# Kernel optimization log

Hardware: AMD Instinct MI355X
Metric: run time of the kernel (lower is better)

The kernel has to match this reference:

```python
import jax, jax.numpy as jnp
import numpy as np
from jax import lax

B, C, T, D, H, W = 1, 8, 8, 24, 48, 48
KT = 3  # temporal kernel taps (module's time loop == valid forward conv, stride 1, pad 0)
KS = 3  # spatial kernel size
S = 2   # spatial stride of the transposed conv
P = 1   # spatial padding of the transposed conv


def setup_inputs() -> dict:
    key = jax.random.key(0)
    kx, kw = jax.random.split(key)
    x = jax.random.normal(kx, (B, C, T, D, H, W), dtype=jnp.float32)
    # torch layout (out_channels, in_channels, kT, kD, kH, kW); the module assigns the
    # slice weight[:, :, i] directly as ConvTranspose3d.weight, so at runtime dim0 acts
    # as the transpose-conv INPUT-channel dim (works because in_ch == out_ch).
    fan_in = C * KT * KS ** 3
    bound = float(1.0 / np.sqrt(fan_in))
    weight = jax.random.uniform(kw, (C, C, KT, KS, KS, KS), dtype=jnp.float32,
                                minval=-bound, maxval=bound)
    return {"x": x, "weight": weight}


def _convT3d(x5, wt):
    # x5: [N, Cin, D, H, W]; wt: ConvTranspose3d weight laid out [Cin, Cout, kD, kH, kW].
    # Transposed conv == forward conv with spatially flipped kernel, swapped I/O dims,
    # lhs dilation = stride, per-side padding = dil*(k-1) - p.
    rhs = jnp.flip(wt, axis=(2, 3, 4)).transpose(1, 0, 2, 3, 4)  # [Cout, Cin, k, k, k]
    pad = KS - 1 - P
    return lax.conv_general_dilated(
        x5, rhs,
        window_strides=(1, 1, 1),
        padding=[(pad, pad)] * 3,
        lhs_dilation=(S, S, S),
        dimension_numbers=("NCDHW", "OIDHW", "NCDHW"))


def reference(x, weight):
    b, c, t = x.shape[:3]
    t_o = t - (KT - 1)  # temporal valid forward conv: out[f] = sum_i conv_i(x[f + i])
    # fold time into batch so each temporal tap is a single big 3D conv
    xr = x.transpose(0, 2, 1, 3, 4, 5).reshape(b * t, c, *x.shape[3:])
    out = None
    for i in range(KT):  # small fixed loop over kernel taps
        y = _convT3d(xr, weight[:, :, i])                 # [b*t, C, Do, Ho, Wo]
        y = y.reshape(b, t, *y.shape[1:])[:, i:i + t_o]   # frames x[f+i] -> out[f]
        out = y if out is None else out + y
    return out.transpose(0, 2, 1, 3, 4, 5)  # [B, C, t_o, Do, Ho, Wo]
```

## Files before the change

kernel.cpp:

```cpp
#include <hip/hip_runtime.h>


typedef float  f32x4  __attribute__((ext_vector_type(4)));
typedef float  f4a    __attribute__((ext_vector_type(4)));
typedef short  bf16x8 __attribute__((ext_vector_type(8)));
typedef unsigned int u32;
typedef u32    u32x4  __attribute__((ext_vector_type(4)));

namespace {
constexpr int T_ = 8, D_ = 24, H_ = 48, W_ = 48;
constexpr int TO = 6, DO_ = 47, HO = 95, WO = 95;
constexpr int XCS = T_ * D_ * H_ * W_;
constexpr int XFS = D_ * H_ * W_;
constexpr int XDS = H_ * W_;
constexpr long OCS = (long)TO * DO_ * HO * WO;
constexpr int OFS = DO_ * HO * WO;
constexpr int ODS = HO * WO;

constexpr int AG[4] = {24, 12, 12, 8};
constexpr int AOFF[4] = {0, 3072, 4608, 6144};
constexpr int LSTR = 48;

__global__ __launch_bounds__(256) void pack_kernel(const float* __restrict__ w,
                                                   unsigned short* __restrict__ A) {
  const int tid = blockIdx.x * 256 + threadIdx.x;
  const int nthr = gridDim.x * 256;
  const int NDs[4] = {2, 2, 1, 1}, NHs[4] = {2, 1, 2, 1}, KR[4] = {192, 96, 96, 48};
  for (int c = 0; c < 4; ++c) {
    const int cnt = AG[c] * 128;
    for (int e = tid; e < cnt; e += nthr) {
      const int j = e & 7, r = (e >> 3) & 15, g = e >> 7;
      const int k = g * 8 + j;
      float v = 0.f;
      if (k < KR[c]) {
        int gg, a = 0, b = 0, cc;
        if (c == 0)      { gg = g;                a = (j >> 2) & 1; b = (j >> 1) & 1; cc = j & 1; }
        else if (c == 1) { gg = 2 * g + (j >> 2); a = (j >> 1) & 1;                   cc = j & 1; }
        else if (c == 2) { gg = 2 * g + (j >> 2); b = (j >> 1) & 1;                   cc = j & 1; }
        else             { gg = 4 * g + (j >> 1);                                     cc = j & 1; }
        if (gg < 24) {
          const int ci = gg / 3, i = gg - 3 * (gg / 3);
          const int kd = (NDs[c] == 2) ? (a ? 2 : 0) : 1;
          const int kh = (NHs[c] == 2) ? (b ? 2 : 0) : 1;
          const int co = r & 7;
          int kw = (r < 8) ? (cc == 0 ? 1 : -1) : (cc == 0 ? 2 : 0);
          if (kw >= 0) v = w[ci * 648 + co * 81 + i * 27 + kd * 9 + kh * 3 + kw];
        }
      }
      u32 u = __float_as_uint(v);
      u += 0x7FFFu + ((u >> 16) & 1u);
      A[AOFF[c] + e] = (unsigned short)(u >> 16);
    }
  }
}

template<int PD, int PH>
__device__ __forceinline__ void wave_body(
    const u32* __restrict__ lds, const unsigned short* __restrict__ A,
    float* __restrict__ out, int f, int od, int oh, int ihb, int lane)
{
  constexpr int CLS = (PD && PH) ? 0 : PD ? 1 : PH ? 2 : 3;
  constexpr int NSTEP = (CLS == 0) ? 6 : (CLS == 3) ? 2 : 3;
  const int c15 = lane & 15, q = lane >> 4;
  const int th = ((oh + PH) >> 1) - ihb;

  bf16x8 af[NSTEP];
  {
    const unsigned short* Ap = A + AOFF[CLS] + c15 * 8;
    #pragma unroll
    for (int s = 0; s < NSTEP; ++s)
      af[s] = *reinterpret_cast<const bf16x8*>(Ap + (s * 4 + q) * 128);
  }

  f32x4 acc[3];
  #pragma unroll
  for (int b = 0; b < 3; ++b) acc[b] = {0, 0, 0, 0};

  #pragma unroll
  for (int blk = 0; blk < 3; ++blk) {
    const int n = blk * 16 + c15;
    #pragma unroll
    for (int s = 0; s < NSTEP; ++s) {
      const int G = s * 4 + q;
      const u32* base;
      int o0, o1, o2, o3;
      if constexpr (CLS == 0) {
        base = lds + (G * 6 + th - 1) * LSTR + n;
        o0 = 1; o1 = 0; o2 = 4; o3 = 3;
      } else if constexpr (CLS == 1) {
        base = lds + (2 * G * 6 + th) * LSTR + n;
        o0 = 0; o1 = 3; o2 = 6; o3 = 9;
      } else if constexpr (CLS == 2) {
        base = lds + (2 * G * 6 + 3 + th - 1) * LSTR + n;
        o0 = 1; o1 = 0; o2 = 7; o3 = 6;
      } else {
        const int g4 = (G > 5) ? 20 : 4 * G;
        base = lds + (g4 * 6 + 3 + th) * LSTR + n;
        o0 = 0; o1 = 6; o2 = 12; o3 = 18;
      }
      const u32x4 ue = {base[o0 * LSTR], base[o1 * LSTR], base[o2 * LSTR], base[o3 * LSTR]};
      acc[blk] = __builtin_amdgcn_mfma_f32_16x16x32_bf16(af[s], __builtin_bit_cast(bf16x8, ue), acc[blk], 0, 0, 0);
    }
  }

  const int isO = (q >= 2);
  const int co0 = (q & 1) * 4;
  #pragma unroll
  for (int blk = 0; blk < 3; ++blk) {
    const int ow = blk * 32 + 2 * c15 + isO;
    if (ow < 95) {
      const long ob = (long)f * OFS + (long)od * ODS + (long)oh * HO + ow;
      #pragma unroll
      for (int j = 0; j < 4; ++j)
        out[(long)(co0 + j) * OCS + ob] = acc[blk][j];
    }
  }
}

constexpr int NBLK = 6 * 24 * 24;

__global__ __launch_bounds__(512) void convt4d_kernel(
    const float* __restrict__ x, const unsigned short* __restrict__ A,
    float* __restrict__ out)
{
  __shared__ u32 lds[144 * LSTR];

  constexpr int qq = NBLK / 8;
  const int bid = blockIdx.x;
  const int L = (bid & 7) * qq + (bid >> 3);
  const int og = L % 24;
  const int rest = L / 24;
  const int odp = rest % 24, f = rest / 24;

  const int tid = threadIdx.x;
  const int ihb = og * 2;
  const int idp = odp + 1;

  for (int c = tid; c < 144 * 12; c += 512) {
    const int row = c / 12, ch = c % 12;
    const int t = row % 3;
    const int r2 = row / 3;
    const int e = r2 & 1;
    const int r3 = r2 >> 1;
    const int i = r3 % 3, ci = r3 / 3;
    int plane = idp - e; if (plane > 23) plane = 23;
    int ih = ihb + t; if (ih > 47) ih = 47;
    const float* src = x + ci * XCS + (f + i) * XFS + plane * XDS + ih * W_ + ch * 4;
    const f4a v = *reinterpret_cast<const f4a*>(src);
    const float v4 = (ch == 11) ? 0.f : src[4];
    const u32 b0 = __float_as_uint(v.x), b1 = __float_as_uint(v.y);
    const u32 b2 = __float_as_uint(v.z), b3 = __float_as_uint(v.w);
    const u32 b4 = __float_as_uint(v4);
    const u32x4 pk = {__builtin_amdgcn_perm(b1, b0, 0x07060302u),
                      __builtin_amdgcn_perm(b2, b1, 0x07060302u),
                      __builtin_amdgcn_perm(b3, b2, 0x07060302u),
                      __builtin_amdgcn_perm(b4, b3, 0x07060302u)};
    *reinterpret_cast<u32x4*>(&lds[row * LSTR + ch * 4]) = pk;
  }
  __syncthreads();

  const int w = tid >> 6, lane = tid & 63;
  const int half = w >> 2;
  const int od = 2 * odp + half;
  if (od > 46) return;
  int oh = og * 4 + (w & 3);
  if (oh > 94) oh = 93;
  if (half) {
    if (oh & 1) wave_body<1, 1>(lds, A, out, f, od, oh, ihb, lane);
    else        wave_body<1, 0>(lds, A, out, f, od, oh, ihb, lane);
  } else {
    if (oh & 1) wave_body<0, 1>(lds, A, out, f, od, oh, ihb, lane);
    else        wave_body<0, 0>(lds, A, out, f, od, oh, ihb, lane);
  }
}
}

extern "C" void kernel_launch(void* const* d_in, const int* in_sizes, int n_in,
                              void* d_out, int out_size, void* d_ws, size_t ws_size,
                              hipStream_t stream) {
  const float* x = (const float*)d_in[0];
  const float* w = (const float*)d_in[1];
  float* out = (float*)d_out;
  unsigned short* A = (unsigned short*)d_ws;
  hipLaunchKernelGGL(pack_kernel, dim3(8), dim3(256), 0, stream, w, A);
  hipLaunchKernelGGL(convt4d_kernel, dim3(NBLK), dim3(512), 0, stream, x, A, out);
}
```

Before: 35.68 us.

## Transpose LDS tile to column-major so MFMA B-operand gathers use wider loads

Stores the bf16-packed input tile in LDS column-major (column stride 146) instead of row-major with stride 48. Rows are reordered and the weight packing's kd/kh order is permuted to match, so the four u32 words each lane gathers per MFMA step are contiguous or close together. For two of the four output-parity classes this lets the compiler issue two 64-bit LDS reads instead of four scalar reads. The cost is that the fill loop now does four scalar strided LDS writes instead of one 128-bit write, and bank conflicts change with the odd-ish stride.

```diff
diff --git a/kernel.cpp b/kernel.cpp
--- a/kernel.cpp
+++ b/kernel.cpp
@@ -5,6 +5,7 @@
 typedef float  f4a    __attribute__((ext_vector_type(4)));
 typedef short  bf16x8 __attribute__((ext_vector_type(8)));
 typedef unsigned int u32;
+typedef u32    u32x2  __attribute__((ext_vector_type(2)));
 typedef u32    u32x4  __attribute__((ext_vector_type(4)));
 
 namespace {
@@ -19,13 +20,13 @@
 
 constexpr int AG[4] = {24, 12, 12, 8};
 constexpr int AOFF[4] = {0, 3072, 4608, 6144};
-constexpr int LSTR = 48;
+constexpr int NRSTR = 146;
 
 __global__ __launch_bounds__(256) void pack_kernel(const float* __restrict__ w,
                                                    unsigned short* __restrict__ A) {
   const int tid = blockIdx.x * 256 + threadIdx.x;
   const int nthr = gridDim.x * 256;
-  const int NDs[4] = {2, 2, 1, 1}, NHs[4] = {2, 1, 2, 1}, KR[4] = {192, 96, 96, 48};
+  const int KR[4] = {192, 96, 96, 48};
   for (int c = 0; c < 4; ++c) {
     const int cnt = AG[c] * 128;
     for (int e = tid; e < cnt; e += nthr) {
@@ -33,15 +34,14 @@
       const int k = g * 8 + j;
       float v = 0.f;
       if (k < KR[c]) {
-        int gg, a = 0, b = 0, cc;
-        if (c == 0)      { gg = g;                a = (j >> 2) & 1; b = (j >> 1) & 1; cc = j & 1; }
-        else if (c == 1) { gg = 2 * g + (j >> 2); a = (j >> 1) & 1;                   cc = j & 1; }
-        else if (c == 2) { gg = 2 * g + (j >> 2); b = (j >> 1) & 1;                   cc = j & 1; }
-        else             { gg = 4 * g + (j >> 1);                                     cc = j & 1; }
-        if (gg < 24) {
+        int gg = -1, kd = 1, kh = 1;
+        const int cc = j & 1;
+        if (c == 0)      { gg = g;               kd = ((j >> 1) & 1) ? 2 : 0; kh = ((j >> 2) & 1) ? 0 : 2; }
+        else if (c == 1) { gg = 2 * g + (j >> 2); kd = ((j >> 1) & 1) ? 2 : 0; kh = 1; }
+        else if (c == 2) { gg = 2 * g + (j >> 2); kd = 1; kh = ((j >> 1) & 1) ? 0 : 2; }
+        else             { gg = 4 * g + (j >> 1); kd = 1; kh = 1; }
+        if (gg >= 0 && gg < 24) {
           const int ci = gg / 3, i = gg - 3 * (gg / 3);
-          const int kd = (NDs[c] == 2) ? (a ? 2 : 0) : 1;
-          const int kh = (NHs[c] == 2) ? (b ? 2 : 0) : 1;
           const int co = r & 7;
           int kw = (r < 8) ? (cc == 0 ? 1 : -1) : (cc == 0 ? 2 : 0);
           if (kw >= 0) v = w[ci * 648 + co * 81 + i * 27 + kd * 9 + kh * 3 + kw];
@@ -79,26 +79,29 @@
   #pragma unroll
   for (int blk = 0; blk < 3; ++blk) {
     const int n = blk * 16 + c15;
+    const u32* col = lds + n * NRSTR;
     #pragma unroll
     for (int s = 0; s < NSTEP; ++s) {
       const int G = s * 4 + q;
-      const u32* base;
-      int o0, o1, o2, o3;
+      u32x4 ue;
       if constexpr (CLS == 0) {
-        base = lds + (G * 6 + th - 1) * LSTR + n;
-        o0 = 1; o1 = 0; o2 = 4; o3 = 3;
+        const u32* b = col + G * 6 + 2 * th - 2;
+        const u32x2 lo = *reinterpret_cast<const u32x2*>(b);
+        const u32x2 hi = *reinterpret_cast<const u32x2*>(b + 2);
+        ue = u32x4{lo.x, lo.y, hi.x, hi.y};
       } else if constexpr (CLS == 1) {
-        base = lds + (2 * G * 6 + th) * LSTR + n;
-        o0 = 0; o1 = 3; o2 = 6; o3 = 9;
+        const u32* b = col + 2 * G * 6 + 2 * th;
+        const u32x2 lo = *reinterpret_cast<const u32x2*>(b);
+        const u32x2 hi = *reinterpret_cast<const u32x2*>(b + 6);
+        ue = u32x4{lo.x, lo.y, hi.x, hi.y};
       } else if constexpr (CLS == 2) {
-        base = lds + (2 * G * 6 + 3 + th - 1) * LSTR + n;
-        o0 = 1; o1 = 0; o2 = 7; o3 = 6;
+        const u32* b = col + 2 * G * 6 + 2 * th - 1;
+        ue = u32x4{b[0], b[2], b[6], b[8]};
       } else {
         const int g4 = (G > 5) ? 20 : 4 * G;
-        base = lds + (g4 * 6 + 3 + th) * LSTR + n;
-        o0 = 0; o1 = 6; o2 = 12; o3 = 18;
+        const u32* b = col + g4 * 6 + 2 * th + 1;
+        ue = u32x4{b[0], b[6], b[12], b[18]};
       }
-      const u32x4 ue = {base[o0 * LSTR], base[o1 * LSTR], base[o2 * LSTR], base[o3 * LSTR]};
       acc[blk] = __builtin_amdgcn_mfma_f32_16x16x32_bf16(af[s], __builtin_bit_cast(bf16x8, ue), acc[blk], 0, 0, 0);
     }
   }
@@ -123,7 +126,7 @@
     const float* __restrict__ x, const unsigned short* __restrict__ A,
     float* __restrict__ out)
 {
-  __shared__ u32 lds[144 * LSTR];
+  __shared__ u32 lds[48 * NRSTR];
 
   constexpr int qq = NBLK / 8;
   const int bid = blockIdx.x;
@@ -138,11 +141,10 @@
 
   for (int c = tid; c < 144 * 12; c += 512) {
     const int row = c / 12, ch = c % 12;
-    const int t = row % 3;
-    const int r2 = row / 3;
-    const int e = r2 & 1;
-    const int r3 = r2 >> 1;
-    const int i = r3 % 3, ci = r3 / 3;
+    const int gg = row / 6;
+    const int rem = row % 6;
+    const int t = rem >> 1, e = rem & 1;
+    const int i = gg % 3, ci = gg / 3;
     int plane = idp - e; if (plane > 23) plane = 23;
     int ih = ihb + t; if (ih > 47) ih = 47;
     const float* src = x + ci * XCS + (f + i) * XFS + plane * XDS + ih * W_ + ch * 4;
@@ -151,11 +153,11 @@
     const u32 b0 = __float_as_uint(v.x), b1 = __float_as_uint(v.y);
     const u32 b2 = __float_as_uint(v.z), b3 = __float_as_uint(v.w);
     const u32 b4 = __float_as_uint(v4);
-    const u32x4 pk = {__builtin_amdgcn_perm(b1, b0, 0x07060302u),
-                      __builtin_amdgcn_perm(b2, b1, 0x07060302u),
-                      __builtin_amdgcn_perm(b3, b2, 0x07060302u),
-                      __builtin_amdgcn_perm(b4, b3, 0x07060302u)};
-    *reinterpret_cast<u32x4*>(&lds[row * LSTR + ch * 4]) = pk;
+    u32* dst = lds + (4 * ch) * NRSTR + row;
+    dst[0 * NRSTR] = __builtin_amdgcn_perm(b1, b0, 0x07060302u);
+    dst[1 * NRSTR] = __builtin_amdgcn_perm(b2, b1, 0x07060302u);
+    dst[2 * NRSTR] = __builtin_amdgcn_perm(b3, b2, 0x07060302u);
+    dst[3 * NRSTR] = __builtin_amdgcn_perm(b4, b3, 0x07060302u);
   }
   __syncthreads();
 
```

Result: no change. 35.73 us (+0.1%).
